# Kernel tuning notes

Measured on AMD Instinct MI355X. Metric: run time of the kernel, lower is better.

Reference implementation:

```python
import jax, jax.numpy as jnp
import numpy as np
from jax import lax

EPS = 1e-5  # BatchNorm eps (inference mode)

def _bn(x, g, b, m, v):
    # inference batchnorm over channel axis 1 of NCHW
    s = g / jnp.sqrt(v + EPS)
    return x * s[None, :, None, None] + (b - m * s)[None, :, None, None]

def _conv1x1(w, x):
    # w: [O, C], x: [B, C, H, W]
    return jnp.einsum('oc,bchw->bohw', w, x)

def setup_inputs() -> dict:
    key = jax.random.key(0)
    ks = jax.random.split(key, 40)
    B, Cin, S = 8, 2048, 64
    R, D, H, NC = 128, 512, 64, 19
    f32 = jnp.float32
    def n(k, shape, scale):
        return jax.random.normal(k, shape, dtype=f32) * scale
    inp = {}
    inp['x'] = jax.random.normal(ks[0], (B, Cin, S, S), f32)
    inp['feat_w'] = n(ks[1], (D, Cin, 3, 3), 0.02)
    # 4 batchnorms: feat, encoding, fusion, conv6
    for i, name in enumerate(['bn1', 'bn2', 'bn3', 'bn4']):
        kk = jax.random.split(ks[2 + i], 4)
        inp[name + '_g'] = jax.random.uniform(kk[0], (D,), f32, 0.5, 1.5)
        inp[name + '_b'] = n(kk[1], (D,), 0.05)
        inp[name + '_m'] = n(kk[2], (D,), 0.1)
        inp[name + '_v'] = jax.random.uniform(kk[3], (D,), f32, 0.5, 1.5)
    inp['enc_w'] = n(ks[6], (D, D), 0.05)
    inp['fc_w'] = n(ks[7], (D, D), 0.05)
    inp['fc_b'] = n(ks[8], (D,), 0.05)
    inp['w1'] = n(ks[9], (R, D, D), 0.05)   # conv1_1[i]: 512->512 1x1
    inp['w2'] = n(ks[10], (R, H, H), 0.05)  # conv1_2[i]: 64->64 1x1
    inp['w3'] = n(ks[11], (R, H, H), 0.05)  # conv1_3[i]: 64->64 1x1
    inp['fusion_w'] = n(ks[12], (D, D), 0.05)
    inp['c6a_w'] = n(ks[13], (D, 2 * D), 0.05)
    inp['c6b_w'] = n(ks[14], (NC, D), 0.05)
    inp['c6b_b'] = n(ks[15], (NC,), 0.05)
    return inp

def reference(x, feat_w,
              bn1_g, bn1_b, bn1_m, bn1_v,
              bn2_g, bn2_b, bn2_m, bn2_v,
              bn3_g, bn3_b, bn3_m, bn3_v,
              bn4_g, bn4_b, bn4_m, bn4_v,
              enc_w, fc_w, fc_b, w1, w2, w3,
              fusion_w, c6a_w, c6b_w, c6b_b):
    # self.feat: 3x3 conv -> BN -> ReLU
    feat = jax.nn.relu(_bn(
        lax.conv_general_dilated(x, feat_w, (1, 1), 'SAME',
                                 dimension_numbers=('NCHW', 'OIHW', 'NCHW')),
        bn1_g, bn1_b, bn1_m, bn1_v))

    # EncModule (se_loss=False)
    enc = jax.nn.relu(_bn(_conv1x1(enc_w, feat), bn2_g, bn2_b, bn2_m, bn2_v))
    en = enc.mean(axis=(2, 3))                                # [B, 512]
    gamma = jax.nn.sigmoid(en @ fc_w.T + fc_b)                # [B, 512]
    se_out = jax.nn.relu(feat * (1.0 + gamma[:, :, None, None]))

    # ContextDecomp: pooled mode vectors (AdaptiveAvgPool2d(1) of permutes)
    Cvec = feat.mean(axis=(2, 3))   # [B, 512] channel vector
    Hvec = feat.mean(axis=(1, 2))   # [B, 64]  (avg over channel & height -> width axis)
    Wvec = feat.mean(axis=(1, 3))   # [B, 64]  (avg over channel & width  -> height axis)
    # all 128 rank-wise 1x1 convs + sigmoid, batched over rank r
    CC = jax.nn.sigmoid(jnp.einsum('roc,bc->bro', w1, Cvec))  # [B, R, 512]
    HH = jax.nn.sigmoid(jnp.einsum('roh,bh->bro', w2, Hvec))  # [B, R, 64]
    WW = jax.nn.sigmoid(jnp.einsum('row,bw->bro', w3, Wvec))  # [B, R, 64]
    # Tucker/CP reconstruction summed over ranks; torch layout puts the
    # width-derived vector (HH) on spatial axis 2 and height-derived (WW) on axis 3
    t1 = jnp.einsum('brc,bri,brj->bcij', CC, HH, WW) * 0.015625  # 1/64
    t = feat * (1.0 + t1)
    outs = jax.nn.relu(_bn(_conv1x1(fusion_w, t), bn3_g, bn3_b, bn3_m, bn3_v))

    # conv6 head: cat -> 1x1 conv -> BN -> ReLU -> (dropout eval=id) -> 1x1 conv
    cat = jnp.concatenate([outs, se_out], axis=1)              # [B, 1024, 64, 64]
    h6 = jax.nn.relu(_bn(_conv1x1(c6a_w, cat), bn4_g, bn4_b, bn4_m, bn4_v))
    out = _conv1x1(c6b_w, h6) + c6b_b[None, :, None, None]     # [B, 19, 64, 64]
    return out
```

## Files before the change

### kernel.cpp

```cpp
#include <hip/hip_runtime.h>
#include <stdint.h>
#include <stddef.h>

using u16 = unsigned short;
using u32 = unsigned int;

typedef __attribute__((ext_vector_type(8))) short short8;
typedef __attribute__((ext_vector_type(4))) float f32x4;

#define DEV static __device__ __forceinline__

DEV float bf2f(u16 v){ union{u32 u; float f;} x; x.u = ((u32)v)<<16; return x.f; }
DEV u16 f2bf(float f){ union{float f; u32 u;} x; x.f = f; u32 r = (x.u + 0x7FFFu + ((x.u>>16)&1u))>>16; return (u16)r; }
DEV float lo16(u32 u){ union{u32 u; float f;} x; x.u = u<<16; return x.f; }
DEV float hi16(u32 u){ union{u32 u; float f;} x; x.u = u & 0xFFFF0000u; return x.f; }

DEV void gload16(const u16* g, u16* l){
  __builtin_amdgcn_global_load_lds((const __attribute__((address_space(1))) void*)g,
                                   (__attribute__((address_space(3))) void*)l, 16, 0, 0);
}

#define BAR    __builtin_amdgcn_s_barrier()
#define SCHED0 __builtin_amdgcn_sched_barrier(0)
#define PRIO1  __builtin_amdgcn_s_setprio(1)
#define PRIO0  __builtin_amdgcn_s_setprio(0)
#define VMC4   asm volatile("s_waitcnt vmcnt(4)" ::: "memory")

__global__ __launch_bounds__(512, 2)
void conv_gemm256(const u16* __restrict__ xp, const u16* __restrict__ wt,
                  u16* __restrict__ O, const float* __restrict__ sb)
{
  constexpr int NT = 288;
  __shared__ u16 smA[2*256*64];
  __shared__ u16 smB[2*256*64];
  const int t = threadIdx.x;
  const int lane = t & 63;
  const int wv = t >> 6;
  const int wr = wv >> 2, wc = wv & 3;
  const int mt = blockIdx.x, nt = blockIdx.y, b = blockIdx.z;
  const int ij0 = mt*256, n0 = nt*256;
  const u16* Ab = xp + (size_t)b*66*66*2048;

  const int tA   = t >> 3;
  const int sc8  = ((t&7) ^ ((t>>3)&7)) * 8;
  const int ldsc = (t&7) * 8;
  const int qB   = t >> 8;
  const int rB   = (t>>3) & 31;

  f32x4 acc[8][4];
  #pragma unroll
  for (int i=0;i<8;++i)
    #pragma unroll
    for (int j=0;j<4;++j) acc[i][j] = (f32x4){0.f,0.f,0.f,0.f};

  short8 aR[4][2];
  short8 bR[2][2][2];

#define STG_A(dst, s, kt_) do{ \
    const int ktc = (kt_) < NT ? (kt_) : (NT-1); \
    const int tap = ktc>>5; const int ty = (tap*11)>>5; const int tx = tap - ty*3; \
    const size_t ko = ((size_t)(ktc&31))<<6; \
    _Pragma("unroll") for (int l=0;l<2;++l){ \
      const int row = (s)*64 + tA + l*128; \
      const u16* src = Ab + ((size_t)((mt*4 + (s) + l*2 + ty)*66 + tA + tx))*2048 + ko + sc8; \
      gload16(src, (dst) + row*64 + ldsc); } }while(0)

#define STG_B(dst, s, kt_) do{ \
    const int ktc = (kt_) < NT ? (kt_) : (NT-1); \
    const int tap = ktc>>5; \
    const size_t ko = (size_t)tap*2048 + (((size_t)(ktc&31))<<6); \
    _Pragma("unroll") for (int l=0;l<2;++l){ \
      const int row = (l*2 + qB)*64 + (s)*32 + rB; \
      const u16* src = wt + ((size_t)(n0 + row))*9*2048 + ko + sc8; \
      gload16(src, (dst) + row*64 + ldsc); } }while(0)

#define LDA_(base, mh) do{ _Pragma("unroll") for(int mi=0;mi<4;++mi){ \
    const int r = wr*128 + (mh)*64 + mi*16 + (lane&15); \
    _Pragma("unroll") for(int kk=0;kk<2;++kk){ \
      const int ch = (kk*4 + (lane>>4)) ^ (r&7); \
      aR[mi][kk] = *(const short8*)&(base)[r*64 + ch*8]; } } }while(0)
#define LDB_(base, nh) do{ _Pragma("unroll") for(int ni=0;ni<2;++ni){ \
    const int r = wc*64 + (nh)*32 + ni*16 + (lane&15); \
    _Pragma("unroll") for(int kk=0;kk<2;++kk){ \
      const int ch = (kk*4 + (lane>>4)) ^ (r&7); \
      bR[nh][ni][kk] = *(const short8*)&(base)[r*64 + ch*8]; } } }while(0)
#define MFMAQ(mh, nh) do{ _Pragma("unroll") for(int mi=0;mi<4;++mi) \
    _Pragma("unroll") for(int ni=0;ni<2;++ni){ \
      acc[(mh)*4+mi][(nh)*2+ni] = __builtin_amdgcn_mfma_f32_16x16x32_bf16(aR[mi][0], bR[nh][ni][0], acc[(mh)*4+mi][(nh)*2+ni],0,0,0); \
      acc[(mh)*4+mi][(nh)*2+ni] = __builtin_amdgcn_mfma_f32_16x16x32_bf16(aR[mi][1], bR[nh][ni][1], acc[(mh)*4+mi][(nh)*2+ni],0,0,0); } }while(0)

  STG_A(smA, 0, 0);
  STG_B(smB, 0, 0);
  STG_B(smB, 1, 0);
  STG_A(smA, 1, 0);
  VMC4;
  BAR; SCHED0;

  for (int j=0; j<NT; ++j) {
    const int p = j & 1;
    const u16* As = smA + (p<<14);
    const u16* Bs = smB + (p<<14);
    u16* Aalt = smA + ((p^1)<<14);
    u16* Balt = smB + ((p^1)<<14);

    LDA_(As, 0); LDB_(Bs, 0);
    STG_A(Aalt, 0, j+1);
    BAR; SCHED0;
    PRIO1; MFMAQ(0,0); PRIO0;
    VMC4;
    BAR; SCHED0;

    LDB_(Bs, 1);
    STG_B(Balt, 0, j+1);
    BAR; SCHED0;
    PRIO1; MFMAQ(0,1); PRIO0;
    VMC4;
    BAR; SCHED0;

    LDA_(As, 1);
    STG_B(Balt, 1, j+1);
    BAR; SCHED0;
    PRIO1; MFMAQ(1,0); PRIO0;
    BAR; SCHED0;

    STG_A(Aalt, 1, j+1);
    BAR; SCHED0;
    PRIO1; MFMAQ(1,1); PRIO0;
    VMC4;
    BAR; SCHED0;
  }

  #pragma unroll
  for (int n=0; n<4; ++n) {
    const int col = n0 + wc*64 + (n>>1)*32 + (n&1)*16 + (lane&15);
    const float s = sb[col], bb = sb[512+col];
    #pragma unroll
    for (int a=0; a<8; ++a) {
      const int row0 = ij0 + wr*128 + (a>>2)*64 + (a&3)*16 + ((lane>>4)<<2);
      #pragma unroll
      for (int j2=0; j2<4; ++j2) {
        const size_t idx = ((size_t)(b*4096 + row0 + j2))*512 + col;
        float v = acc[a][n][j2]*s + bb;
        O[idx] = f2bf(v > 0.f ? v : 0.f);
      }
    }
  }
#undef STG_A
#undef STG_B
#undef LDA_
#undef LDB_
#undef MFMAQ
}

template<int V>
__global__ __launch_bounds__(256)
void gemm128(const u16* __restrict__ A, const u16* __restrict__ Bw, u16* __restrict__ O,
             const u16* __restrict__ feat, const u16* __restrict__ B2,
             const float* __restrict__ sb, float* __restrict__ en)
{
  constexpr int NSEG = (V==4)?2:1;
  constexpr int KSEG = (V==2)?128:512;
  __shared__ u16 smA[128*64];
  __shared__ u16 smB[128*64];
  const int tid = threadIdx.x;
  const int lane = tid & 63;
  const int wv = tid >> 6;
  const int wr = wv >> 1, wc = wv & 1;
  const int mt = blockIdx.x, nt = blockIdx.y, b = blockIdx.z;
  const int ij0 = mt*128, n0 = nt*128;
  const int srow = tid >> 3, schunk = tid & 7;

  f32x4 acc[4][4];
  #pragma unroll
  for (int i=0;i<4;++i)
    #pragma unroll
    for (int j=0;j<4;++j) acc[i][j] = (f32x4){0.f,0.f,0.f,0.f};

  for (int seg=0; seg<NSEG; ++seg) {
    const u16* Ab;
    const u16* Bb;
    if constexpr (V==1 || V==3) { Ab = A + (size_t)b*4096*512; Bb = Bw; }
    else if constexpr (V==2) { Ab = A + (size_t)b*4096*128; Bb = Bw + (size_t)b*512*128; }
    else { Ab = (seg==0 ? A : feat) + (size_t)b*4096*512;
           Bb = (seg==0) ? Bw : (B2 + (size_t)b*512*512); }

    for (int kt=0; kt<KSEG/64; ++kt) {
      const int k0 = kt*64;
      #pragma unroll
      for (int i=0;i<4;++i) {
        const int row = i*32 + srow;
        const int sc = schunk ^ (row & 7);
        const u16* src;
        if constexpr (V==2) src = Ab + (size_t)(ij0+row)*128 + (k0 + sc*8);
        else                src = Ab + (size_t)(ij0+row)*512 + (k0 + sc*8);
        gload16(src, &smA[row*64 + schunk*8]);
      }
      #pragma unroll
      for (int i=0;i<4;++i) {
        const int row = i*32 + srow;
        const int sc = schunk ^ (row & 7);
        const int o = n0 + row;
        const u16* src;
        if constexpr (V==2) src = Bb + (size_t)o*128 + (k0 + sc*8);
        else                src = Bb + (size_t)o*512 + (k0 + sc*8);
        gload16(src, &smB[row*64 + schunk*8]);
      }
      __syncthreads();
      #pragma unroll
      for (int ks=0; ks<2; ++ks) {
        short8 av[4], bv[4];
        #pragma unroll
        for (int mi=0;mi<4;++mi) {
          const int r = wr*64 + mi*16 + (lane & 15);
          const int ch = (ks*4 + (lane>>4)) ^ (r & 7);
          av[mi] = *(const short8*)&smA[r*64 + ch*8];
        }
        #pragma unroll
        for (int ni=0;ni<4;++ni) {
          const int r = wc*64 + ni*16 + (lane & 15);
          const int ch = (ks*4 + (lane>>4)) ^ (r & 7);
          bv[ni] = *(const short8*)&smB[r*64 + ch*8];
        }
        #pragma unroll
        for (int mi=0;mi<4;++mi)
          #pragma unroll
          for (int ni=0;ni<4;++ni)
            acc[mi][ni] = __builtin_amdgcn_mfma_f32_16x16x32_bf16(av[mi], bv[ni], acc[mi][ni], 0, 0, 0);
      }
      __syncthreads();
    }
  }

  if constexpr (V==1) {
    #pragma unroll
    for (int ni=0;ni<4;++ni) {
      const int col = n0 + wc*64 + ni*16 + (lane & 15);
      const float s = sb[col], bb = sb[512+col];
      float cs = 0.f;
      #pragma unroll
      for (int mi=0;mi<4;++mi)
        #pragma unroll
        for (int j=0;j<4;++j) {
          float v = acc[mi][ni][j]*s + bb;
          cs += (v > 0.f) ? v : 0.f;
        }
      cs += __shfl_xor(cs, 16);
      cs += __shfl_xor(cs, 32);
      if (lane < 16) atomicAdd(&en[b*512 + col], cs * (1.0f/4096.0f));
    }
  } else {
    #pragma unroll
    for (int ni=0;ni<4;++ni) {
      const int col = n0 + wc*64 + ni*16 + (lane & 15);
      float s = 0.f, bb = 0.f;
      if constexpr (V!=2) { s = sb[col]; bb = sb[512+col]; }
      #pragma unroll
      for (int mi=0;mi<4;++mi) {
        const int row0 = ij0 + wr*64 + mi*16 + ((lane>>4)<<2);
        #pragma unroll
        for (int j=0;j<4;++j) {
          const size_t idx = ((size_t)(b*4096 + row0 + j))*512 + col;
          float v = acc[mi][ni][j];
          if constexpr (V==2) {
            O[idx] = f2bf(bf2f(feat[idx]) * (1.0f + v));
          } else {
            v = v*s + bb;
            O[idx] = f2bf(v > 0.f ? v : 0.f);
          }
        }
      }
    }
  }
}

__global__ __launch_bounds__(256)
void prep_weights(const float* __restrict__ fw, const float* __restrict__ encw,
                  const float* __restrict__ fusw, const float* __restrict__ c6aw,
                  u16* __restrict__ wt, u16* __restrict__ encb,
                  u16* __restrict__ fusb, u16* __restrict__ c6a1)
{
  const int bx = blockIdx.x, t = threadIdx.x;
  if (bx < 512) {
    const int o = bx;
    for (int c = t; c < 2048; c += 256) {
      const float* src = fw + ((size_t)o*2048 + c)*9;
      #pragma unroll
      for (int tt=0; tt<9; ++tt)
        wt[((size_t)o*9 + tt)*2048 + c] = f2bf(src[tt]);
    }
  } else if (bx < 1536) {
    const int i = (bx-512)*256 + t;
    encb[i] = f2bf(encw[i]);
  } else if (bx < 2560) {
    const int i = (bx-1536)*256 + t;
    fusb[i] = f2bf(fusw[i]);
  } else {
    const int i = (bx-2560)*256 + t;
    c6a1[i] = f2bf(c6aw[(size_t)(i>>9)*1024 + (i&511)]);
  }
}

__global__ void bn_prep(const float* g1,const float* b1,const float* m1,const float* v1,
                        const float* g2,const float* b2,const float* m2,const float* v2,
                        const float* g3,const float* b3,const float* m3,const float* v3,
                        const float* g4,const float* b4,const float* m4,const float* v4,
                        float* __restrict__ bnsb)
{
  const int c = blockIdx.x*256 + threadIdx.x;
  if (c >= 512) return;
  const float eps = 1e-5f;
  float s1 = g1[c]*rsqrtf(v1[c]+eps); bnsb[c]      = s1; bnsb[512+c]  = b1[c]-m1[c]*s1;
  float s2 = g2[c]*rsqrtf(v2[c]+eps); bnsb[1024+c] = s2; bnsb[1536+c] = b2[c]-m2[c]*s2;
  float s3 = g3[c]*rsqrtf(v3[c]+eps); bnsb[2048+c] = s3; bnsb[2560+c] = b3[c]-m3[c]*s3;
  float s4 = g4[c]*rsqrtf(v4[c]+eps); bnsb[3072+c] = s4; bnsb[3584+c] = b4[c]-m4[c]*s4;
}

__global__ __launch_bounds__(256)
void pad_x(const float* __restrict__ x, u16* __restrict__ xp)
{
  __shared__ u16 tile[256*66];
  const int bx = blockIdx.x;
  const int cb = bx & 7, y = (bx>>3) & 63, b = bx >> 9;
  const int t = threadIdx.x;
  const int xcol = t & 63, crow = t >> 6;
  for (int it=0; it<64; ++it) {
    const int cl = it*4 + crow;
    tile[cl*66 + xcol] = f2bf(x[(((size_t)b*2048 + cb*256 + cl)*64 + y)*64 + xcol]);
  }
  __syncthreads();
  const size_t rowbase = (size_t)(b*66 + y + 1)*66;
  for (int px=0; px<64; ++px)
    xp[(rowbase + px + 1)*2048 + cb*256 + t] = tile[t*66 + px];
  xp[rowbase*2048 + cb*256 + t] = 0;
  xp[(rowbase + 65)*2048 + cb*256 + t] = 0;
  if (y == 0) {
    const size_t rb = (size_t)(b*66)*66;
    for (int px=0; px<66; ++px) xp[(rb+px)*2048 + cb*256 + t] = 0;
  }
  if (y == 63) {
    const size_t rb = (size_t)(b*66 + 65)*66;
    for (int px=0; px<66; ++px) xp[(rb+px)*2048 + cb*256 + t] = 0;
  }
}

__global__ __launch_bounds__(256)
void reduce_feat(const u16* __restrict__ feat, float* __restrict__ Cvec,
                 float* __restrict__ Hvec, float* __restrict__ Wvec)
{
  __shared__ float cbuf[4*512];
  const int bx = blockIdx.x;
  const int y = bx & 63, b = bx >> 6;
  const int t = threadIdx.x, lane = t & 63, wv = t >> 6;
  const int c0 = lane*8;
  float cs[8] = {0,0,0,0,0,0,0,0};
  float wsum = 0.f;
  for (int xx = wv; xx < 64; xx += 4) {
    const u16* p = feat + ((size_t)(b*4096 + y*64 + xx))*512 + c0;
    const uint4 d = *(const uint4*)p;
    const float f0=lo16(d.x),f1=hi16(d.x),f2=lo16(d.y),f3=hi16(d.y),
                f4=lo16(d.z),f5=hi16(d.z),f6=lo16(d.w),f7=hi16(d.w);
    cs[0]+=f0; cs[1]+=f1; cs[2]+=f2; cs[3]+=f3; cs[4]+=f4; cs[5]+=f5; cs[6]+=f6; cs[7]+=f7;
    float xs = ((f0+f1)+(f2+f3)) + ((f4+f5)+(f6+f7));
    #pragma unroll
    for (int off=32; off; off>>=1) xs += __shfl_xor(xs, off);
    if (lane == 0) { atomicAdd(&Hvec[b*64 + xx], xs*(1.0f/32768.0f)); wsum += xs; }
  }
  if (lane == 0) atomicAdd(&Wvec[b*64 + y], wsum*(1.0f/32768.0f));
  #pragma unroll
  for (int j=0;j<8;++j) cbuf[wv*512 + c0 + j] = cs[j];
  __syncthreads();
  for (int c=t; c<512; c+=256) {
    const float s = cbuf[c] + cbuf[512+c] + cbuf[1024+c] + cbuf[1536+c];
    atomicAdd(&Cvec[b*512 + c], s*(1.0f/4096.0f));
  }
}

__global__ __launch_bounds__(256)
void small1(const float* __restrict__ en, const float* __restrict__ fcw, const float* __restrict__ fcb,
            const float* __restrict__ w1, const float* __restrict__ Cvec,
            const float* __restrict__ w2, const float* __restrict__ w3,
            const float* __restrict__ Hvec, const float* __restrict__ Wvec,
            float* __restrict__ gamma, u16* __restrict__ CCT,
            float* __restrict__ HH, float* __restrict__ WW)
{
  const int bx = blockIdx.x, t = threadIdx.x;
  if (bx < 8) {
    __shared__ float enl[512];
    const int b = bx;
    for (int c=t;c<512;c+=256) enl[c] = en[b*512+c];
    __syncthreads();
    for (int o=t;o<512;o+=256) {
      float a = fcb[o];
      const float* wr = fcw + (size_t)o*512;
      for (int c=0;c<512;++c) a += enl[c]*wr[c];
      gamma[b*512+o] = 1.0f/(1.0f+__expf(-a));
    }
  } else if (bx < 136) {
    __shared__ float hl[512], wl[512];
    const int r = bx - 8;
    for (int i=t;i<512;i+=256){ hl[i]=Hvec[i]; wl[i]=Wvec[i]; }
    __syncthreads();
    const int i = t & 63, bh = t >> 6;
    for (int bb=bh; bb<8; bb+=4) {
      float sh=0.f, sw=0.f;
      const float* w2r = w2 + ((size_t)r*64 + i)*64;
      const float* w3r = w3 + ((size_t)r*64 + i)*64;
      #pragma unroll 8
      for (int h=0;h<64;++h){ sh += w2r[h]*hl[bb*64+h]; sw += w3r[h]*wl[bb*64+h]; }
      HH[((size_t)bb*128 + r)*64 + i] = 1.0f/(1.0f+__expf(-sh));
      WW[((size_t)bb*128 + r)*64 + i] = 1.0f/(1.0f+__expf(-sw));
    }
  } else {
    __shared__ float cv[4096];
    for (int i=t;i<4096;i+=256) cv[i] = Cvec[i];
    __syncthreads();
    const int p = (bx-136)*4 + (t>>6);
    const int r = p >> 9, o = p & 511;
    const int lane = t & 63;
    float ab[8] = {0,0,0,0,0,0,0,0};
    const float* w1r = w1 + ((size_t)r*512 + o)*512;
    #pragma unroll
    for (int it=0; it<8; ++it) {
      const float wvv = w1r[it*64 + lane];
      #pragma unroll
      for (int bb=0;bb<8;++bb) ab[bb] += wvv * cv[bb*512 + it*64 + lane];
    }
    #pragma unroll
    for (int off=32; off; off>>=1)
      #pragma unroll
      for (int bb=0;bb<8;++bb) ab[bb] += __shfl_xor(ab[bb], off);
    #pragma unroll
    for (int bb=0;bb<8;++bb)
      if (lane == bb)
        CCT[((size_t)bb*512 + o)*128 + r] = f2bf((1.0f/(1.0f+__expf(-ab[bb]))) * 0.015625f);
  }
}

__global__ __launch_bounds__(256)
void small2(const float* __restrict__ c6aw, const float* __restrict__ gamma,
            const float* __restrict__ HH, const float* __restrict__ WW,
            u16* __restrict__ w2b, u16* __restrict__ HWT)
{
  const int bx = blockIdx.x, t = threadIdx.x;
  if (bx < 4096) {
    const int b = bx >> 9, o = bx & 511;
    const float* src = c6aw + (size_t)o*1024 + 512;
    const float* gmv = gamma + b*512;
    u16* dst = w2b + ((size_t)b*512 + o)*512;
    for (int c=t;c<512;c+=256) dst[c] = f2bf(src[c]*(1.0f+gmv[c]));
  } else {
    __shared__ float wwl[64*129];
    __shared__ float hhy[128];
    const int idx = bx - 4096;
    const int b = idx >> 6, y = idx & 63;
    for (int g=t; g<8192; g+=256){ const int r=g>>6, xx=g&63; wwl[xx*129+r] = WW[((size_t)b*128+r)*64+xx]; }
    if (t < 128) hhy[t] = HH[((size_t)b*128 + t)*64 + y];
    __syncthreads();
    const int r2 = (t & 63)*2, xg = t >> 6;
    for (int xx=xg; xx<64; xx+=4) {
      const float v0 = hhy[r2]   * wwl[xx*129 + r2];
      const float v1 = hhy[r2+1] * wwl[xx*129 + r2 + 1];
      const u32 pk = (u32)f2bf(v0) | ((u32)f2bf(v1)<<16);
      *(u32*)&HWT[((size_t)(b*4096 + y*64 + xx))*128 + r2] = pk;
    }
  }
}

__global__ __launch_bounds__(256)
void c6b_head(const u16* __restrict__ h6, const float* __restrict__ w,
              const float* __restrict__ bias, float* __restrict__ out)
{
  const int gid = blockIdx.x*256 + threadIdx.x;
  const int b = gid >> 12, ij = gid & 4095;
  float acc[19];
  #pragma unroll
  for (int o=0;o<19;++o) acc[o] = bias[o];
  const u16* hp = h6 + (size_t)gid*512;
  for (int c0=0;c0<512;c0+=8) {
    const uint4 d = *(const uint4*)(hp + c0);
    const float f0=lo16(d.x),f1=hi16(d.x),f2=lo16(d.y),f3=hi16(d.y),
                f4=lo16(d.z),f5=hi16(d.z),f6=lo16(d.w),f7=hi16(d.w);
    #pragma unroll
    for (int o=0;o<19;++o) {
      const float* wr = w + o*512 + c0;
      acc[o] += f0*wr[0] + f1*wr[1] + f2*wr[2] + f3*wr[3]
              + f4*wr[4] + f5*wr[5] + f6*wr[6] + f7*wr[7];
    }
  }
  #pragma unroll
  for (int o=0;o<19;++o) out[((size_t)(b*19 + o))*4096 + ij] = acc[o];
}

extern "C" void kernel_launch(void* const* d_in, const int* in_sizes, int n_in,
                              void* d_out, int out_size, void* d_ws, size_t ws_size,
                              hipStream_t stream)
{
  (void)in_sizes; (void)n_in; (void)out_size;
  const float* x     = (const float*)d_in[0];
  const float* fw    = (const float*)d_in[1];
  const float* bnp[16];
  for (int i=0;i<16;++i) bnp[i] = (const float*)d_in[2+i];
  const float* enc_w = (const float*)d_in[18];
  const float* fc_w  = (const float*)d_in[19];
  const float* fc_b  = (const float*)d_in[20];
  const float* w1    = (const float*)d_in[21];
  const float* w2    = (const float*)d_in[22];
  const float* w3    = (const float*)d_in[23];
  const float* fus_w = (const float*)d_in[24];
  const float* c6a_w = (const float*)d_in[25];
  const float* c6b_w = (const float*)d_in[26];
  const float* c6b_b = (const float*)d_in[27];

  char* ws = (char*)d_ws;
  constexpr size_t OFF_XP=0, OFF_T=0, OFF_OUTS=33554432ull, OFF_H6=67108864ull,
    OFF_WT=142737408ull, OFF_FEAT=161611776ull, OFF_HWT=195166208ull, OFF_W2B=203554816ull,
    OFF_CCT=207749120ull, OFF_ENCB=208797696ull, OFF_FUSB=209321984ull, OFF_C6A1=209846272ull,
    OFF_HH=210370560ull, OFF_WW=210632704ull, OFF_EN=210894848ull, OFF_CV=210911232ull,
    OFF_HV=210927616ull, OFF_WV=210929664ull, OFF_GAMMA=210931712ull, OFF_BNSB=210948096ull,
    NEEDED=210964480ull;
  if (ws_size < NEEDED) return;

  u16* xp    = (u16*)(ws + OFF_XP);
  u16* tb    = (u16*)(ws + OFF_T);
  u16* outs  = (u16*)(ws + OFF_OUTS);
  u16* h6    = (u16*)(ws + OFF_H6);
  u16* wt    = (u16*)(ws + OFF_WT);
  u16* featb = (u16*)(ws + OFF_FEAT);
  u16* hwt   = (u16*)(ws + OFF_HWT);
  u16* w2b   = (u16*)(ws + OFF_W2B);
  u16* cct   = (u16*)(ws + OFF_CCT);
  u16* encb  = (u16*)(ws + OFF_ENCB);
  u16* fusb  = (u16*)(ws + OFF_FUSB);
  u16* c6a1  = (u16*)(ws + OFF_C6A1);
  float* HH  = (float*)(ws + OFF_HH);
  float* WW  = (float*)(ws + OFF_WW);
  float* en  = (float*)(ws + OFF_EN);
  float* Cv  = (float*)(ws + OFF_CV);
  float* Hv  = (float*)(ws + OFF_HV);
  float* Wv  = (float*)(ws + OFF_WV);
  float* gm  = (float*)(ws + OFF_GAMMA);
  float* bnsb= (float*)(ws + OFF_BNSB);

  hipMemsetAsync(ws + OFF_EN, 0, 36864, stream);

  prep_weights<<<3584,256,0,stream>>>(fw, enc_w, fus_w, c6a_w, wt, encb, fusb, c6a1);
  bn_prep<<<2,256,0,stream>>>(bnp[0],bnp[1],bnp[2],bnp[3], bnp[4],bnp[5],bnp[6],bnp[7],
                              bnp[8],bnp[9],bnp[10],bnp[11], bnp[12],bnp[13],bnp[14],bnp[15], bnsb);
  pad_x<<<4096,256,0,stream>>>(x, xp);
  conv_gemm256<<<dim3(16,2,8),512,0,stream>>>(xp, wt, featb, bnsb);
  reduce_feat<<<512,256,0,stream>>>(featb, Cv, Hv, Wv);
  gemm128<1><<<dim3(32,4,8),256,0,stream>>>(featb, encb, nullptr, nullptr, nullptr, bnsb+1024, en);
  small1<<<16520,256,0,stream>>>(en, fc_w, fc_b, w1, Cv, w2, w3, Hv, Wv, gm, cct, HH, WW);
  small2<<<4608,256,0,stream>>>(c6a_w, gm, HH, WW, w2b, hwt);
  gemm128<2><<<dim3(32,4,8),256,0,stream>>>(hwt, cct, tb, featb, nullptr, nullptr, nullptr);
  gemm128<3><<<dim3(32,4,8),256,0,stream>>>(tb, fusb, outs, nullptr, nullptr, bnsb+2048, nullptr);
  gemm128<4><<<dim3(32,4,8),256,0,stream>>>(outs, c6a1, h6, featb, w2b, bnsb+3072, nullptr);
  c6b_head<<<128,256,0,stream>>>(h6, c6b_w, c6b_b, (float*)d_out);
}
```

Measured before the change: 998.5 us.

## Fuse feature mean reductions into conv epilogue and merge BN prep into weight prep

The channel, height and width mean reductions of the conv output are now computed in the conv GEMM epilogue. Each thread accumulates partial sums, reduces them with wave shuffles and LDS atomics, then issues global atomics, which removes the separate reduce_feat kernel that re-read the 32MB feature map. The bn_prep kernel is folded into prep_weights as two extra blocks, saving one launch. The cost is extra epilogue work and atomics in the register-heavy conv kernel, plus a possible change in register pressure.

```diff
diff --git a/kernel.cpp b/kernel.cpp
--- a/kernel.cpp
+++ b/kernel.cpp
@@ -25,10 +25,13 @@
 #define PRIO1  __builtin_amdgcn_s_setprio(1)
 #define PRIO0  __builtin_amdgcn_s_setprio(0)
 #define VMC4   asm volatile("s_waitcnt vmcnt(4)" ::: "memory")
+#define VMC0   asm volatile("s_waitcnt vmcnt(0)" ::: "memory")
 
 __global__ __launch_bounds__(512, 2)
 void conv_gemm256(const u16* __restrict__ xp, const u16* __restrict__ wt,
-                  u16* __restrict__ O, const float* __restrict__ sb)
+                  u16* __restrict__ O, const float* __restrict__ sb,
+                  float* __restrict__ Cvec, float* __restrict__ Hvec,
+                  float* __restrict__ Wvec)
 {
   constexpr int NT = 288;
   __shared__ u16 smA[2*256*64];
@@ -130,10 +133,25 @@
     BAR; SCHED0;
   }
 
+  VMC0;
+  BAR;
+  float* red = (float*)smA;
+  if (t < 324) red[t] = 0.f;
+  BAR;
+
+  float xs[4][4];
+  #pragma unroll
+  for (int q=0;q<4;++q)
+    #pragma unroll
+    for (int j2=0;j2<4;++j2) xs[q][j2] = 0.f;
+  float ys0 = 0.f, ys1 = 0.f;
+
   #pragma unroll
   for (int n=0; n<4; ++n) {
-    const int col = n0 + wc*64 + (n>>1)*32 + (n&1)*16 + (lane&15);
+    const int cloc = wc*64 + (n>>1)*32 + (n&1)*16 + (lane&15);
+    const int col = n0 + cloc;
     const float s = sb[col], bb = sb[512+col];
+    float cs = 0.f;
     #pragma unroll
     for (int a=0; a<8; ++a) {
       const int row0 = ij0 + wr*128 + (a>>2)*64 + (a&3)*16 + ((lane>>4)<<2);
@@ -141,10 +159,38 @@
       for (int j2=0; j2<4; ++j2) {
         const size_t idx = ((size_t)(b*4096 + row0 + j2))*512 + col;
         float v = acc[a][n][j2]*s + bb;
-        O[idx] = f2bf(v > 0.f ? v : 0.f);
+        v = v > 0.f ? v : 0.f;
+        O[idx] = f2bf(v);
+        cs += v;
+        xs[a&3][j2] += v;
+        if (a < 4) ys0 += v; else ys1 += v;
       }
     }
-  }
+    atomicAdd(&red[cloc], cs);
+  }
+  #pragma unroll
+  for (int off=1; off<16; off<<=1)
+    #pragma unroll
+    for (int q=0;q<4;++q)
+      #pragma unroll
+      for (int j2=0;j2<4;++j2) xs[q][j2] += __shfl_xor(xs[q][j2], off);
+  if ((lane & 15) == 0) {
+    #pragma unroll
+    for (int q=0;q<4;++q)
+      #pragma unroll
+      for (int j2=0;j2<4;++j2)
+        atomicAdd(&red[256 + q*16 + (lane>>4)*4 + j2], xs[q][j2]);
+  }
+  #pragma unroll
+  for (int off=1; off<64; off<<=1) { ys0 += __shfl_xor(ys0, off); ys1 += __shfl_xor(ys1, off); }
+  if (lane == 0) {
+    atomicAdd(&red[320 + wr*2 + 0], ys0);
+    atomicAdd(&red[320 + wr*2 + 1], ys1);
+  }
+  BAR;
+  if (t < 256)       atomicAdd(&Cvec[b*512 + n0 + t], red[t]*(1.0f/4096.0f));
+  else if (t < 320)  atomicAdd(&Hvec[b*64 + (t-256)], red[t]*(1.0f/32768.0f));
+  else if (t < 324)  atomicAdd(&Wvec[b*64 + (ij0>>6) + (t-320)], red[t]*(1.0f/32768.0f));
 #undef STG_A
 #undef STG_B
 #undef LDA_
@@ -276,8 +322,13 @@
 __global__ __launch_bounds__(256)
 void prep_weights(const float* __restrict__ fw, const float* __restrict__ encw,
                   const float* __restrict__ fusw, const float* __restrict__ c6aw,
+                  const float* g1,const float* b1,const float* m1,const float* v1,
+                  const float* g2,const float* b2,const float* m2,const float* v2,
+                  const float* g3,const float* b3,const float* m3,const float* v3,
+                  const float* g4,const float* b4,const float* m4,const float* v4,
                   u16* __restrict__ wt, u16* __restrict__ encb,
-                  u16* __restrict__ fusb, u16* __restrict__ c6a1)
+                  u16* __restrict__ fusb, u16* __restrict__ c6a1,
+                  float* __restrict__ bnsb)
 {
   const int bx = blockIdx.x, t = threadIdx.x;
   if (bx < 512) {
@@ -294,25 +345,19 @@
   } else if (bx < 2560) {
     const int i = (bx-1536)*256 + t;
     fusb[i] = f2bf(fusw[i]);
-  } else {
+  } else if (bx < 3584) {
     const int i = (bx-2560)*256 + t;
     c6a1[i] = f2bf(c6aw[(size_t)(i>>9)*1024 + (i&511)]);
-  }
-}
-
-__global__ void bn_prep(const float* g1,const float* b1,const float* m1,const float* v1,
-                        const float* g2,const float* b2,const float* m2,const float* v2,
-                        const float* g3,const float* b3,const float* m3,const float* v3,
-                        const float* g4,const float* b4,const float* m4,const float* v4,
-                        float* __restrict__ bnsb)
-{
-  const int c = blockIdx.x*256 + threadIdx.x;
-  if (c >= 512) return;
-  const float eps = 1e-5f;
-  float s1 = g1[c]*rsqrtf(v1[c]+eps); bnsb[c]      = s1; bnsb[512+c]  = b1[c]-m1[c]*s1;
-  float s2 = g2[c]*rsqrtf(v2[c]+eps); bnsb[1024+c] = s2; bnsb[1536+c] = b2[c]-m2[c]*s2;
-  float s3 = g3[c]*rsqrtf(v3[c]+eps); bnsb[2048+c] = s3; bnsb[2560+c] = b3[c]-m3[c]*s3;
-  float s4 = g4[c]*rsqrtf(v4[c]+eps); bnsb[3072+c] = s4; bnsb[3584+c] = b4[c]-m4[c]*s4;
+  } else {
+    const int c = (bx-3584)*256 + t;
+    if (c < 512) {
+      const float eps = 1e-5f;
+      float s1 = g1[c]*rsqrtf(v1[c]+eps); bnsb[c]      = s1; bnsb[512+c]  = b1[c]-m1[c]*s1;
+      float s2 = g2[c]*rsqrtf(v2[c]+eps); bnsb[1024+c] = s2; bnsb[1536+c] = b2[c]-m2[c]*s2;
+      float s3 = g3[c]*rsqrtf(v3[c]+eps); bnsb[2048+c] = s3; bnsb[2560+c] = b3[c]-m3[c]*s3;
+      float s4 = g4[c]*rsqrtf(v4[c]+eps); bnsb[3072+c] = s4; bnsb[3584+c] = b4[c]-m4[c]*s4;
+    }
+  }
 }
 
 __global__ __launch_bounds__(256)
@@ -340,38 +385,6 @@
   if (y == 63) {
     const size_t rb = (size_t)(b*66 + 65)*66;
     for (int px=0; px<66; ++px) xp[(rb+px)*2048 + cb*256 + t] = 0;
-  }
-}
-
-__global__ __launch_bounds__(256)
-void reduce_feat(const u16* __restrict__ feat, float* __restrict__ Cvec,
-                 float* __restrict__ Hvec, float* __restrict__ Wvec)
-{
-  __shared__ float cbuf[4*512];
-  const int bx = blockIdx.x;
-  const int y = bx & 63, b = bx >> 6;
-  const int t = threadIdx.x, lane = t & 63, wv = t >> 6;
-  const int c0 = lane*8;
-  float cs[8] = {0,0,0,0,0,0,0,0};
-  float wsum = 0.f;
-  for (int xx = wv; xx < 64; xx += 4) {
-    const u16* p = feat + ((size_t)(b*4096 + y*64 + xx))*512 + c0;
-    const uint4 d = *(const uint4*)p;
-    const float f0=lo16(d.x),f1=hi16(d.x),f2=lo16(d.y),f3=hi16(d.y),
-                f4=lo16(d.z),f5=hi16(d.z),f6=lo16(d.w),f7=hi16(d.w);
-    cs[0]+=f0; cs[1]+=f1; cs[2]+=f2; cs[3]+=f3; cs[4]+=f4; cs[5]+=f5; cs[6]+=f6; cs[7]+=f7;
-    float xs = ((f0+f1)+(f2+f3)) + ((f4+f5)+(f6+f7));
-    #pragma unroll
-    for (int off=32; off; off>>=1) xs += __shfl_xor(xs, off);
-    if (lane == 0) { atomicAdd(&Hvec[b*64 + xx], xs*(1.0f/32768.0f)); wsum += xs; }
-  }
-  if (lane == 0) atomicAdd(&Wvec[b*64 + y], wsum*(1.0f/32768.0f));
-  #pragma unroll
-  for (int j=0;j<8;++j) cbuf[wv*512 + c0 + j] = cs[j];
-  __syncthreads();
-  for (int c=t; c<512; c+=256) {
-    const float s = cbuf[c] + cbuf[512+c] + cbuf[1024+c] + cbuf[1536+c];
-    atomicAdd(&Cvec[b*512 + c], s*(1.0f/4096.0f));
   }
 }
 
@@ -543,12 +556,12 @@
 
   hipMemsetAsync(ws + OFF_EN, 0, 36864, stream);
 
-  prep_weights<<<3584,256,0,stream>>>(fw, enc_w, fus_w, c6a_w, wt, encb, fusb, c6a1);
-  bn_prep<<<2,256,0,stream>>>(bnp[0],bnp[1],bnp[2],bnp[3], bnp[4],bnp[5],bnp[6],bnp[7],
-                              bnp[8],bnp[9],bnp[10],bnp[11], bnp[12],bnp[13],bnp[14],bnp[15], bnsb);
+  prep_weights<<<3586,256,0,stream>>>(fw, enc_w, fus_w, c6a_w,
+      bnp[0],bnp[1],bnp[2],bnp[3], bnp[4],bnp[5],bnp[6],bnp[7],
+      bnp[8],bnp[9],bnp[10],bnp[11], bnp[12],bnp[13],bnp[14],bnp[15],
+      wt, encb, fusb, c6a1, bnsb);
   pad_x<<<4096,256,0,stream>>>(x, xp);
-  conv_gemm256<<<dim3(16,2,8),512,0,stream>>>(xp, wt, featb, bnsb);
-  reduce_feat<<<512,256,0,stream>>>(featb, Cv, Hv, Wv);
+  conv_gemm256<<<dim3(16,2,8),512,0,stream>>>(xp, wt, featb, bnsb, Cv, Hv, Wv);
   gemm128<1><<<dim3(32,4,8),256,0,stream>>>(featb, encb, nullptr, nullptr, nullptr, bnsb+1024, en);
   small1<<<16520,256,0,stream>>>(en, fc_w, fc_b, w1, Cv, w2, w3, Hv, Wv, gm, cct, HH, WW);
   small2<<<4608,256,0,stream>>>(c6a_w, gm, HH, WW, w2b, hwt);
```

Measured after the change: 965.0 us. -3.3%, faster.
